# Performance work log

Measured on AMD Instinct MI355X. Metric: run time of the kernel, lower is better.

The kernel has to match this reference:

```python
import jax, jax.numpy as jnp
import numpy as np

N, IN, HID, H, OUT = 5000, 64, 32, 4, 64
NEG_SLOPE = 0.2  # LeakyReLU slope used by GAT
MASK_VAL = -1e9


def setup_inputs() -> dict:
    key = jax.random.key(0)
    ks = jax.random.split(key, 8)
    adj = (jax.random.uniform(ks[0], (N, N)) < 0.02).astype(jnp.float32)
    adj = jnp.maximum(adj, jnp.eye(N, dtype=jnp.float32))
    h = jax.random.normal(ks[1], (N, IN), dtype=jnp.float32)
    # layer 1 params: W1 [IN, H*HID], attention vectors a1_* [H, HID]
    W1 = jax.random.normal(ks[2], (IN, H * HID), dtype=jnp.float32) / np.sqrt(IN)
    a1_src = jax.random.normal(ks[3], (H, HID), dtype=jnp.float32) / np.sqrt(HID)
    a1_dst = jax.random.normal(ks[4], (H, HID), dtype=jnp.float32) / np.sqrt(HID)
    # layer 2 params: single head, W2 [H*HID, OUT]
    W2 = jax.random.normal(ks[5], (H * HID, OUT), dtype=jnp.float32) / np.sqrt(H * HID)
    a2_src = jax.random.normal(ks[6], (1, OUT), dtype=jnp.float32) / np.sqrt(OUT)
    a2_dst = jax.random.normal(ks[7], (1, OUT), dtype=jnp.float32) / np.sqrt(OUT)
    return {"adj": adj, "h": h, "W1": W1, "a1_src": a1_src, "a1_dst": a1_dst,
            "W2": W2, "a2_src": a2_src, "a2_dst": a2_dst}


def gat_conv(adj, x, W, a_src, a_dst, heads, out_dim):
    n = x.shape[0]
    Wh = (x @ W).reshape(n, heads, out_dim)              # [N, H, F']
    s_src = jnp.einsum('nhf,hf->nh', Wh, a_src)          # score contribution of node as center i
    s_dst = jnp.einsum('nhf,hf->nh', Wh, a_dst)          # contribution of node as neighbor j
    e = s_src[:, None, :] + s_dst[None, :, :]            # [N, N, H]
    e = jax.nn.leaky_relu(e, NEG_SLOPE)
    e = jnp.where(adj[:, :, None] > 0, e, MASK_VAL)
    alpha = jax.nn.softmax(e, axis=1)                    # softmax over neighbors j
    out = jnp.einsum('ijh,jhf->ihf', alpha, Wh)          # aggregate
    return out.reshape(n, heads * out_dim)               # concat heads


def reference(adj, h, W1, a1_src, a1_dst, W2, a2_src, a2_dst):
    x = gat_conv(adj, h, W1, a1_src, a1_dst, H, HID)     # [N, H*HID]
    x = jax.nn.elu(x)
    out = gat_conv(adj, x, W2, a2_src, a2_dst, 1, OUT)   # [N, OUT]
    return out
```

## Files before the change

kernel.cpp:

```cpp
#include <hip/hip_runtime.h>
#include <math.h>

#define NN   5000
#define INF_ 64
#define HID  32
#define NH   4
#define OUTF 64
#define NEG  0.2f
#define CAP  256

typedef float nt4 __attribute__((ext_vector_type(4)));

__device__ inline float wred_sum(float v) {
#pragma unroll
    for (int off = 32; off > 0; off >>= 1) v += __shfl_down(v, off, 64);
    return v;
}

__global__ __launch_bounds__(256) void k1(const float* __restrict__ adj,
        const float* __restrict__ h, const float* __restrict__ W1,
        const float* __restrict__ a1s, const float* __restrict__ a1d,
        int* __restrict__ counts, int* __restrict__ idx,
        float* __restrict__ Wh1, float* __restrict__ s1s, float* __restrict__ s1d) {
    const int i = blockIdx.x, t = threadIdx.x;
    const int lane = t & 63;
    __shared__ int cnt;
    __shared__ float hs[INF_];
    __shared__ int nbs[CAP];
    if (t == 0) cnt = 0;
    if (t < INF_) hs[t] = h[i * INF_ + t];
    __syncthreads();
    if (t < 128) {
        float acc = 0.f;
#pragma unroll
        for (int k = 0; k < INF_; ++k) acc += hs[k] * W1[k * (NH * HID) + t];
        Wh1[(size_t)i * (NH * HID) + t] = acc;
        const int hd = t >> 5, f = t & 31;
        float vs = acc * a1s[hd * HID + f];
        float vd = acc * a1d[hd * HID + f];
#pragma unroll
        for (int off = 16; off > 0; off >>= 1) {
            vs += __shfl_down(vs, off, 32);
            vd += __shfl_down(vd, off, 32);
        }
        if (f == 0) { s1s[i * NH + hd] = vs; s1d[i * NH + hd] = vd; }
    }
    const nt4* row4 = (const nt4*)(adj + (size_t)i * NN);
    for (int j = t; j < NN / 4; j += 256) {
        nt4 v = __builtin_nontemporal_load(&row4[j]);
        const bool p0 = v.x > 0.f, p1 = v.y > 0.f, p2 = v.z > 0.f, p3 = v.w > 0.f;
        const unsigned long long b0 = __ballot(p0);
        const unsigned long long b1 = __ballot(p1);
        const unsigned long long b2 = __ballot(p2);
        const unsigned long long b3 = __ballot(p3);
        const int t0 = __popcll(b0), t1 = __popcll(b1), t2 = __popcll(b2), t3 = __popcll(b3);
        const int tot = t0 + t1 + t2 + t3;
        int base = 0;
        if (lane == 0 && tot) base = atomicAdd(&cnt, tot);
        base = __builtin_amdgcn_readfirstlane(base);
        const unsigned long long below = (1ull << lane) - 1ull;
        if (p0) { int p = base + __popcll(b0 & below);               if (p < CAP) nbs[p] = 4 * j;     }
        if (p1) { int p = base + t0 + __popcll(b1 & below);          if (p < CAP) nbs[p] = 4 * j + 1; }
        if (p2) { int p = base + t0 + t1 + __popcll(b2 & below);     if (p < CAP) nbs[p] = 4 * j + 2; }
        if (p3) { int p = base + t0 + t1 + t2 + __popcll(b3 & below);if (p < CAP) nbs[p] = 4 * j + 3; }
    }
    __syncthreads();
    const int c = cnt < CAP ? cnt : CAP;
    if (t == 0) counts[i] = c;
    int4* my4 = (int4*)(idx + (size_t)i * CAP);
    const int c4 = (c + 3) >> 2;
    for (int e = t; e < c4; e += 256) my4[e] = ((const int4*)nbs)[e];
}

__global__ __launch_bounds__(256) void k2(const int* __restrict__ counts,
        const int* __restrict__ idx, const float* __restrict__ Wh1,
        const float* __restrict__ s1s, const float* __restrict__ s1d,
        const float* __restrict__ W2, const float* __restrict__ a2s,
        const float* __restrict__ a2d, float* __restrict__ Wh2,
        float* __restrict__ s2s, float* __restrict__ s2d) {
    const int i = blockIdx.x, t = threadIdx.x;
    const int lane = t & 63, wave = t >> 6;
    const int c = counts[i];
    __shared__ int   nb[CAP];
    __shared__ float sc[NH][CAP];
    __shared__ float aggf[4][128];
    __shared__ float xs[128];
    __shared__ float redh[4 * NH];
    __shared__ float pw[4][64];
    const float4 ss = ((const float4*)s1s)[i];
    const float4* s1d4 = (const float4*)s1d;
    const int* my = idx + (size_t)i * CAP;
    float l0 = 0.f, l1 = 0.f, l2 = 0.f, l3 = 0.f;
    for (int e = t; e < c; e += 256) {
        const int j = my[e];
        nb[e] = j;
        const float4 sd = s1d4[j];
        float v0 = ss.x + sd.x, v1 = ss.y + sd.y, v2 = ss.z + sd.z, v3 = ss.w + sd.w;
        v0 = (v0 >= 0.f) ? v0 : NEG * v0;
        v1 = (v1 >= 0.f) ? v1 : NEG * v1;
        v2 = (v2 >= 0.f) ? v2 : NEG * v2;
        v3 = (v3 >= 0.f) ? v3 : NEG * v3;
        const float p0 = __expf(v0), p1 = __expf(v1), p2 = __expf(v2), p3 = __expf(v3);
        sc[0][e] = p0; sc[1][e] = p1; sc[2][e] = p2; sc[3][e] = p3;
        l0 += p0; l1 += p1; l2 += p2; l3 += p3;
    }
    l0 = wred_sum(l0); l1 = wred_sum(l1); l2 = wred_sum(l2); l3 = wred_sum(l3);
    if (lane == 0) {
        redh[wave * NH + 0] = l0; redh[wave * NH + 1] = l1;
        redh[wave * NH + 2] = l2; redh[wave * NH + 3] = l3;
    }
    __syncthreads();
    {
        const float2* Wh1v = (const float2*)Wh1;
        const int hd = lane >> 4;
        const int q = (((c + 3) >> 2) + 3) & ~3;
        const int e0 = wave * q, e1 = min(c, e0 + q);
        float2 a0 = {0.f, 0.f}, a1 = {0.f, 0.f}, a2 = {0.f, 0.f}, a3 = {0.f, 0.f};
        int e = e0;
        for (; e + 3 < e1; e += 4) {
            const int j0 = nb[e], j1 = nb[e + 1], j2 = nb[e + 2], j3 = nb[e + 3];
            const float2 w0 = Wh1v[(size_t)j0 * 64 + lane];
            const float2 w1 = Wh1v[(size_t)j1 * 64 + lane];
            const float2 w2 = Wh1v[(size_t)j2 * 64 + lane];
            const float2 w3 = Wh1v[(size_t)j3 * 64 + lane];
            const float p0 = sc[hd][e], p1 = sc[hd][e + 1], p2 = sc[hd][e + 2], p3 = sc[hd][e + 3];
            a0.x += p0 * w0.x; a0.y += p0 * w0.y;
            a1.x += p1 * w1.x; a1.y += p1 * w1.y;
            a2.x += p2 * w2.x; a2.y += p2 * w2.y;
            a3.x += p3 * w3.x; a3.y += p3 * w3.y;
        }
        for (; e < e1; ++e) {
            const float2 w = Wh1v[(size_t)nb[e] * 64 + lane];
            const float p = sc[hd][e];
            a0.x += p * w.x; a0.y += p * w.y;
        }
        aggf[wave][2 * lane]     = (a0.x + a1.x) + (a2.x + a3.x);
        aggf[wave][2 * lane + 1] = (a0.y + a1.y) + (a2.y + a3.y);
    }
    __syncthreads();
    if (t < 128) {
        const int hh = t >> 5;
        const float lh = redh[hh] + redh[NH + hh] + redh[2 * NH + hh] + redh[3 * NH + hh];
        float o = aggf[0][t] + aggf[1][t] + aggf[2][t] + aggf[3][t];
        o = o / lh;
        o = (o > 0.f) ? o : expm1f(o);
        xs[t] = o;
    }
    __syncthreads();
    {
        float pa = 0.f;
#pragma unroll
        for (int k = 0; k < 32; ++k)
            pa += xs[wave * 32 + k] * W2[(wave * 32 + k) * OUTF + lane];
        pw[wave][lane] = pa;
    }
    __syncthreads();
    if (t < 64) {
        float w = pw[0][t] + pw[1][t] + pw[2][t] + pw[3][t];
        Wh2[(size_t)i * OUTF + t] = w;
        float vs = wred_sum(w * a2s[t]);
        float vd = wred_sum(w * a2d[t]);
        if (t == 0) { s2s[i] = vs; s2d[i] = vd; }
    }
}

__global__ __launch_bounds__(256) void k3(const int* __restrict__ counts,
        const int* __restrict__ idx, const float* __restrict__ Wh2,
        const float* __restrict__ s2s, const float* __restrict__ s2d,
        float* __restrict__ out) {
    const int i = blockIdx.x, t = threadIdx.x;
    const int lane = t & 63, wave = t >> 6;
    const int c = counts[i];
    __shared__ int   nb[CAP];
    __shared__ float sc[CAP];
    __shared__ float red[4];
    __shared__ float agg[4][64];
    const float si = s2s[i];
    const int* my = idx + (size_t)i * CAP;
    float lsum = 0.f;
    for (int e = t; e < c; e += 256) {
        const int j = my[e];
        nb[e] = j;
        float v = si + s2d[j];
        v = (v >= 0.f) ? v : NEG * v;
        const float p = __expf(v);
        sc[e] = p;
        lsum += p;
    }
    lsum = wred_sum(lsum);
    if (lane == 0) red[wave] = lsum;
    __syncthreads();
    const int q = (((c + 3) >> 2) + 3) & ~3;
    const int e0 = wave * q, e1 = min(c, e0 + q);
    float a0 = 0.f, a1 = 0.f, a2 = 0.f, a3 = 0.f;
    int e = e0;
    for (; e + 3 < e1; e += 4) {
        a0 += sc[e]     * Wh2[(size_t)nb[e]     * OUTF + lane];
        a1 += sc[e + 1] * Wh2[(size_t)nb[e + 1] * OUTF + lane];
        a2 += sc[e + 2] * Wh2[(size_t)nb[e + 2] * OUTF + lane];
        a3 += sc[e + 3] * Wh2[(size_t)nb[e + 3] * OUTF + lane];
    }
    for (; e < e1; ++e) a0 += sc[e] * Wh2[(size_t)nb[e] * OUTF + lane];
    agg[wave][lane] = (a0 + a1) + (a2 + a3);
    __syncthreads();
    if (t < 64) {
        const float ls = red[0] + red[1] + red[2] + red[3];
        float s = agg[0][t] + agg[1][t] + agg[2][t] + agg[3][t];
        out[(size_t)i * OUTF + t] = s / ls;
    }
}

extern "C" void kernel_launch(void* const* d_in, const int* in_sizes, int n_in,
                              void* d_out, int out_size, void* d_ws, size_t ws_size,
                              hipStream_t stream) {
    const float* adj = (const float*)d_in[0];
    const float* h   = (const float*)d_in[1];
    const float* W1  = (const float*)d_in[2];
    const float* a1s = (const float*)d_in[3];
    const float* a1d = (const float*)d_in[4];
    const float* W2  = (const float*)d_in[5];
    const float* a2s = (const float*)d_in[6];
    const float* a2d = (const float*)d_in[7];
    float* out = (float*)d_out;

    char* p = (char*)d_ws;
    float* Wh1 = (float*)p; p += (size_t)NN * 128 * 4;
    float* Wh2 = (float*)p; p += (size_t)NN * OUTF * 4;
    float* s1s = (float*)p; p += (size_t)NN * NH * 4;
    float* s1d = (float*)p; p += (size_t)NN * NH * 4;
    float* s2s = (float*)p; p += (size_t)NN * 4;
    float* s2d = (float*)p; p += (size_t)NN * 4;
    int*   cnt = (int*)p;   p += (size_t)NN * 4;
    int*   idx = (int*)p;   p += (size_t)NN * CAP * 4;

    k1<<<NN, 256, 0, stream>>>(adj, h, W1, a1s, a1d, cnt, idx, Wh1, s1s, s1d);
    k2<<<NN, 256, 0, stream>>>(cnt, idx, Wh1, s1s, s1d, W2, a2s, a2d, Wh2, s2s, s2d);
    k3<<<NN, 256, 0, stream>>>(cnt, idx, Wh2, s2s, s2d, out);
}
```

Baseline: 198.1 us.

## Front-load adjacency loads, use prefix-scan compaction, and widen gathers to float4

k1 now issues all five adjacency-row loads per thread up front, before the W1 matvec. It replaces the per-iteration ballot and atomic compaction with a per-thread bitmask plus a wave and block prefix scan. The h row is broadcast through shuffles instead of shared memory. k2 and k3 gather neighbour features as float4, with each half or quarter of a wave handling a different neighbour and a cross-lane reduction at the end; neighbour lists are zero-padded to a multiple of four and k3 drops to 128 threads. This aims to expose more memory parallelism on the dominant adjacency read and cut instruction count in the gathers, at the cost of more registers and a changed load pattern.

```diff
diff --git a/kernel.cpp b/kernel.cpp
--- a/kernel.cpp
+++ b/kernel.cpp
@@ -17,23 +17,32 @@
     return v;
 }
 
+__device__ inline unsigned mask4(nt4 v) {
+    return (v.x > 0.f ? 1u : 0u) | (v.y > 0.f ? 2u : 0u) |
+           (v.z > 0.f ? 4u : 0u) | (v.w > 0.f ? 8u : 0u);
+}
+
 __global__ __launch_bounds__(256) void k1(const float* __restrict__ adj,
         const float* __restrict__ h, const float* __restrict__ W1,
         const float* __restrict__ a1s, const float* __restrict__ a1d,
         int* __restrict__ counts, int* __restrict__ idx,
         float* __restrict__ Wh1, float* __restrict__ s1s, float* __restrict__ s1d) {
     const int i = blockIdx.x, t = threadIdx.x;
-    const int lane = t & 63;
-    __shared__ int cnt;
-    __shared__ float hs[INF_];
+    const int lane = t & 63, wave = t >> 6;
     __shared__ int nbs[CAP];
-    if (t == 0) cnt = 0;
-    if (t < INF_) hs[t] = h[i * INF_ + t];
-    __syncthreads();
+    __shared__ int wt4[4];
+    const nt4* row4 = (const nt4*)(adj + (size_t)i * NN);
+    nt4 v0 = __builtin_nontemporal_load(&row4[t]);
+    nt4 v1 = __builtin_nontemporal_load(&row4[t + 256]);
+    nt4 v2 = __builtin_nontemporal_load(&row4[t + 512]);
+    nt4 v3 = __builtin_nontemporal_load(&row4[t + 768]);
+    nt4 v4 = {0.f, 0.f, 0.f, 0.f};
+    if (t < NN / 4 - 1024) v4 = __builtin_nontemporal_load(&row4[t + 1024]);
+    const float hreg = h[(size_t)i * INF_ + lane];
     if (t < 128) {
         float acc = 0.f;
 #pragma unroll
-        for (int k = 0; k < INF_; ++k) acc += hs[k] * W1[k * (NH * HID) + t];
+        for (int k = 0; k < INF_; ++k) acc += __shfl(hreg, k, 64) * W1[k * (NH * HID) + t];
         Wh1[(size_t)i * (NH * HID) + t] = acc;
         const int hd = t >> 5, f = t & 31;
         float vs = acc * a1s[hd * HID + f];
@@ -45,31 +54,34 @@
         }
         if (f == 0) { s1s[i * NH + hd] = vs; s1d[i * NH + hd] = vd; }
     }
-    const nt4* row4 = (const nt4*)(adj + (size_t)i * NN);
-    for (int j = t; j < NN / 4; j += 256) {
-        nt4 v = __builtin_nontemporal_load(&row4[j]);
-        const bool p0 = v.x > 0.f, p1 = v.y > 0.f, p2 = v.z > 0.f, p3 = v.w > 0.f;
-        const unsigned long long b0 = __ballot(p0);
-        const unsigned long long b1 = __ballot(p1);
-        const unsigned long long b2 = __ballot(p2);
-        const unsigned long long b3 = __ballot(p3);
-        const int t0 = __popcll(b0), t1 = __popcll(b1), t2 = __popcll(b2), t3 = __popcll(b3);
-        const int tot = t0 + t1 + t2 + t3;
-        int base = 0;
-        if (lane == 0 && tot) base = atomicAdd(&cnt, tot);
-        base = __builtin_amdgcn_readfirstlane(base);
-        const unsigned long long below = (1ull << lane) - 1ull;
-        if (p0) { int p = base + __popcll(b0 & below);               if (p < CAP) nbs[p] = 4 * j;     }
-        if (p1) { int p = base + t0 + __popcll(b1 & below);          if (p < CAP) nbs[p] = 4 * j + 1; }
-        if (p2) { int p = base + t0 + t1 + __popcll(b2 & below);     if (p < CAP) nbs[p] = 4 * j + 2; }
-        if (p3) { int p = base + t0 + t1 + t2 + __popcll(b3 & below);if (p < CAP) nbs[p] = 4 * j + 3; }
-    }
-    __syncthreads();
-    const int c = cnt < CAP ? cnt : CAP;
+    const unsigned m20 = mask4(v0) | (mask4(v1) << 4) | (mask4(v2) << 8) |
+                         (mask4(v3) << 12) | (mask4(v4) << 16);
+    const int cl = __popc(m20);
+    int incl = cl;
+#pragma unroll
+    for (int off = 1; off < 64; off <<= 1) {
+        int u = __shfl_up(incl, off, 64);
+        if (lane >= off) incl += u;
+    }
+    if (lane == 63) wt4[wave] = incl;
+    __syncthreads();
+    int base = 0;
+#pragma unroll
+    for (int w = 0; w < 4; ++w) base += (w < wave) ? wt4[w] : 0;
+    int p = base + (incl - cl);
+    unsigned m = m20;
+    while (m) {
+        const int b = __ffs(m) - 1; m &= m - 1;
+        const int nid = 4 * (t + (b >> 2) * 256) + (b & 3);
+        if (p < CAP) nbs[p] = nid;
+        ++p;
+    }
+    __syncthreads();
+    const int tot = wt4[0] + wt4[1] + wt4[2] + wt4[3];
+    const int c = tot < CAP ? tot : CAP;
     if (t == 0) counts[i] = c;
     int4* my4 = (int4*)(idx + (size_t)i * CAP);
-    const int c4 = (c + 3) >> 2;
-    for (int e = t; e < c4; e += 256) my4[e] = ((const int4*)nbs)[e];
+    for (int e = t; e < ((c + 3) >> 2); e += 256) my4[e] = ((const int4*)nbs)[e];
 }
 
 __global__ __launch_bounds__(256) void k2(const int* __restrict__ counts,
@@ -81,8 +93,9 @@
     const int i = blockIdx.x, t = threadIdx.x;
     const int lane = t & 63, wave = t >> 6;
     const int c = counts[i];
+    const int cp = (c + 3) & ~3;
     __shared__ int   nb[CAP];
-    __shared__ float sc[NH][CAP];
+    __shared__ float sc[NH][CAP + 1];
     __shared__ float aggf[4][128];
     __shared__ float xs[128];
     __shared__ float redh[4 * NH];
@@ -95,14 +108,18 @@
         const int j = my[e];
         nb[e] = j;
         const float4 sd = s1d4[j];
-        float v0 = ss.x + sd.x, v1 = ss.y + sd.y, v2 = ss.z + sd.z, v3 = ss.w + sd.w;
-        v0 = (v0 >= 0.f) ? v0 : NEG * v0;
-        v1 = (v1 >= 0.f) ? v1 : NEG * v1;
-        v2 = (v2 >= 0.f) ? v2 : NEG * v2;
-        v3 = (v3 >= 0.f) ? v3 : NEG * v3;
-        const float p0 = __expf(v0), p1 = __expf(v1), p2 = __expf(v2), p3 = __expf(v3);
+        float w0 = ss.x + sd.x, w1 = ss.y + sd.y, w2 = ss.z + sd.z, w3 = ss.w + sd.w;
+        w0 = (w0 >= 0.f) ? w0 : NEG * w0;
+        w1 = (w1 >= 0.f) ? w1 : NEG * w1;
+        w2 = (w2 >= 0.f) ? w2 : NEG * w2;
+        w3 = (w3 >= 0.f) ? w3 : NEG * w3;
+        const float p0 = __expf(w0), p1 = __expf(w1), p2 = __expf(w2), p3 = __expf(w3);
         sc[0][e] = p0; sc[1][e] = p1; sc[2][e] = p2; sc[3][e] = p3;
         l0 += p0; l1 += p1; l2 += p2; l3 += p3;
+    }
+    for (int e = c + t; e < cp; e += 256) {
+        nb[e] = 0;
+        sc[0][e] = 0.f; sc[1][e] = 0.f; sc[2][e] = 0.f; sc[3][e] = 0.f;
     }
     l0 = wred_sum(l0); l1 = wred_sum(l1); l2 = wred_sum(l2); l3 = wred_sum(l3);
     if (lane == 0) {
@@ -111,31 +128,47 @@
     }
     __syncthreads();
     {
-        const float2* Wh1v = (const float2*)Wh1;
-        const int hd = lane >> 4;
-        const int q = (((c + 3) >> 2) + 3) & ~3;
-        const int e0 = wave * q, e1 = min(c, e0 + q);
-        float2 a0 = {0.f, 0.f}, a1 = {0.f, 0.f}, a2 = {0.f, 0.f}, a3 = {0.f, 0.f};
-        int e = e0;
-        for (; e + 3 < e1; e += 4) {
-            const int j0 = nb[e], j1 = nb[e + 1], j2 = nb[e + 2], j3 = nb[e + 3];
-            const float2 w0 = Wh1v[(size_t)j0 * 64 + lane];
-            const float2 w1 = Wh1v[(size_t)j1 * 64 + lane];
-            const float2 w2 = Wh1v[(size_t)j2 * 64 + lane];
-            const float2 w3 = Wh1v[(size_t)j3 * 64 + lane];
-            const float p0 = sc[hd][e], p1 = sc[hd][e + 1], p2 = sc[hd][e + 2], p3 = sc[hd][e + 3];
-            a0.x += p0 * w0.x; a0.y += p0 * w0.y;
-            a1.x += p1 * w1.x; a1.y += p1 * w1.y;
-            a2.x += p2 * w2.x; a2.y += p2 * w2.y;
-            a3.x += p3 * w3.x; a3.y += p3 * w3.y;
+        const float4* Wh1v = (const float4*)Wh1;
+        const int half = lane >> 5, fi = lane & 31, hd = fi >> 3;
+        const int g4 = cp >> 2;
+        const int gw = (g4 + 3) >> 2;
+        int g = wave * gw;
+        const int gend = min(g4, wave * gw + gw);
+        float4 a0 = {0.f,0.f,0.f,0.f}, a1 = a0, a2 = a0, a3 = a0;
+        for (; g + 1 < gend; g += 2) {
+            const int e = 4 * g;
+            const int j0 = nb[e + half],     j1 = nb[e + 2 + half];
+            const int j2 = nb[e + 4 + half], j3 = nb[e + 6 + half];
+            const float p0 = sc[hd][e + half],     p1 = sc[hd][e + 2 + half];
+            const float p2 = sc[hd][e + 4 + half], p3 = sc[hd][e + 6 + half];
+            const float4 w0 = Wh1v[(size_t)j0 * 32 + fi];
+            const float4 w1 = Wh1v[(size_t)j1 * 32 + fi];
+            const float4 w2 = Wh1v[(size_t)j2 * 32 + fi];
+            const float4 w3 = Wh1v[(size_t)j3 * 32 + fi];
+            a0.x += p0 * w0.x; a0.y += p0 * w0.y; a0.z += p0 * w0.z; a0.w += p0 * w0.w;
+            a1.x += p1 * w1.x; a1.y += p1 * w1.y; a1.z += p1 * w1.z; a1.w += p1 * w1.w;
+            a2.x += p2 * w2.x; a2.y += p2 * w2.y; a2.z += p2 * w2.z; a2.w += p2 * w2.w;
+            a3.x += p3 * w3.x; a3.y += p3 * w3.y; a3.z += p3 * w3.z; a3.w += p3 * w3.w;
         }
-        for (; e < e1; ++e) {
-            const float2 w = Wh1v[(size_t)nb[e] * 64 + lane];
-            const float p = sc[hd][e];
-            a0.x += p * w.x; a0.y += p * w.y;
+        if (g < gend) {
+            const int e = 4 * g;
+            const int j0 = nb[e + half], j1 = nb[e + 2 + half];
+            const float p0 = sc[hd][e + half], p1 = sc[hd][e + 2 + half];
+            const float4 w0 = Wh1v[(size_t)j0 * 32 + fi];
+            const float4 w1 = Wh1v[(size_t)j1 * 32 + fi];
+            a0.x += p0 * w0.x; a0.y += p0 * w0.y; a0.z += p0 * w0.z; a0.w += p0 * w0.w;
+            a1.x += p1 * w1.x; a1.y += p1 * w1.y; a1.z += p1 * w1.z; a1.w += p1 * w1.w;
         }
-        aggf[wave][2 * lane]     = (a0.x + a1.x) + (a2.x + a3.x);
-        aggf[wave][2 * lane + 1] = (a0.y + a1.y) + (a2.y + a3.y);
+        float4 aa;
+        aa.x = (a0.x + a1.x) + (a2.x + a3.x);
+        aa.y = (a0.y + a1.y) + (a2.y + a3.y);
+        aa.z = (a0.z + a1.z) + (a2.z + a3.z);
+        aa.w = (a0.w + a1.w) + (a2.w + a3.w);
+        aa.x += __shfl_xor(aa.x, 32, 64);
+        aa.y += __shfl_xor(aa.y, 32, 64);
+        aa.z += __shfl_xor(aa.z, 32, 64);
+        aa.w += __shfl_xor(aa.w, 32, 64);
+        if (lane < 32) ((float4*)aggf[wave])[lane] = aa;
     }
     __syncthreads();
     if (t < 128) {
@@ -164,21 +197,22 @@
     }
 }
 
-__global__ __launch_bounds__(256) void k3(const int* __restrict__ counts,
+__global__ __launch_bounds__(128) void k3(const int* __restrict__ counts,
         const int* __restrict__ idx, const float* __restrict__ Wh2,
         const float* __restrict__ s2s, const float* __restrict__ s2d,
         float* __restrict__ out) {
     const int i = blockIdx.x, t = threadIdx.x;
     const int lane = t & 63, wave = t >> 6;
     const int c = counts[i];
+    const int cp = (c + 3) & ~3;
     __shared__ int   nb[CAP];
     __shared__ float sc[CAP];
-    __shared__ float red[4];
-    __shared__ float agg[4][64];
+    __shared__ float red[2];
+    __shared__ float agg[2][64];
     const float si = s2s[i];
     const int* my = idx + (size_t)i * CAP;
     float lsum = 0.f;
-    for (int e = t; e < c; e += 256) {
+    for (int e = t; e < c; e += 128) {
         const int j = my[e];
         nb[e] = j;
         float v = si + s2d[j];
@@ -187,25 +221,47 @@
         sc[e] = p;
         lsum += p;
     }
+    for (int e = c + t; e < cp; e += 128) { nb[e] = 0; sc[e] = 0.f; }
     lsum = wred_sum(lsum);
     if (lane == 0) red[wave] = lsum;
     __syncthreads();
-    const int q = (((c + 3) >> 2) + 3) & ~3;
-    const int e0 = wave * q, e1 = min(c, e0 + q);
-    float a0 = 0.f, a1 = 0.f, a2 = 0.f, a3 = 0.f;
-    int e = e0;
-    for (; e + 3 < e1; e += 4) {
-        a0 += sc[e]     * Wh2[(size_t)nb[e]     * OUTF + lane];
-        a1 += sc[e + 1] * Wh2[(size_t)nb[e + 1] * OUTF + lane];
-        a2 += sc[e + 2] * Wh2[(size_t)nb[e + 2] * OUTF + lane];
-        a3 += sc[e + 3] * Wh2[(size_t)nb[e + 3] * OUTF + lane];
-    }
-    for (; e < e1; ++e) a0 += sc[e] * Wh2[(size_t)nb[e] * OUTF + lane];
-    agg[wave][lane] = (a0 + a1) + (a2 + a3);
+    const float4* Wh2v = (const float4*)Wh2;
+    const int qi = lane >> 4, fi = lane & 15;
+    const int g4 = cp >> 2;
+    const int gw = (g4 + 1) >> 1;
+    int g = wave * gw;
+    const int gend = min(g4, wave * gw + gw);
+    float4 a0 = {0.f,0.f,0.f,0.f}, a1 = a0;
+    for (; g + 1 < gend; g += 2) {
+        const int eA = 4 * g + qi, eB = 4 * g + 4 + qi;
+        const int jA = nb[eA], jB = nb[eB];
+        const float pA = sc[eA], pB = sc[eB];
+        const float4 wA = Wh2v[(size_t)jA * 16 + fi];
+        const float4 wB = Wh2v[(size_t)jB * 16 + fi];
+        a0.x += pA * wA.x; a0.y += pA * wA.y; a0.z += pA * wA.z; a0.w += pA * wA.w;
+        a1.x += pB * wB.x; a1.y += pB * wB.y; a1.z += pB * wB.z; a1.w += pB * wB.w;
+    }
+    if (g < gend) {
+        const int eA = 4 * g + qi;
+        const int jA = nb[eA];
+        const float pA = sc[eA];
+        const float4 wA = Wh2v[(size_t)jA * 16 + fi];
+        a0.x += pA * wA.x; a0.y += pA * wA.y; a0.z += pA * wA.z; a0.w += pA * wA.w;
+    }
+    float4 aa;
+    aa.x = a0.x + a1.x; aa.y = a0.y + a1.y; aa.z = a0.z + a1.z; aa.w = a0.w + a1.w;
+#pragma unroll
+    for (int off = 16; off <= 32; off <<= 1) {
+        aa.x += __shfl_xor(aa.x, off, 64);
+        aa.y += __shfl_xor(aa.y, off, 64);
+        aa.z += __shfl_xor(aa.z, off, 64);
+        aa.w += __shfl_xor(aa.w, off, 64);
+    }
+    if (lane < 16) ((float4*)agg[wave])[lane] = aa;
     __syncthreads();
     if (t < 64) {
-        const float ls = red[0] + red[1] + red[2] + red[3];
-        float s = agg[0][t] + agg[1][t] + agg[2][t] + agg[3][t];
+        const float ls = red[0] + red[1];
+        const float s = agg[0][t] + agg[1][t];
         out[(size_t)i * OUTF + t] = s / ls;
     }
 }
@@ -235,5 +291,5 @@
 
     k1<<<NN, 256, 0, stream>>>(adj, h, W1, a1s, a1d, cnt, idx, Wh1, s1s, s1d);
     k2<<<NN, 256, 0, stream>>>(cnt, idx, Wh1, s1s, s1d, W2, a2s, a2d, Wh2, s2s, s2d);
-    k3<<<NN, 256, 0, stream>>>(cnt, idx, Wh2, s2s, s2d, out);
-}
+    k3<<<NN, 128, 0, stream>>>(cnt, idx, Wh2, s2s, s2d, out);
+}
```

Result: faster. 189.4 us (-4.4%).
